# Optimization experiments

Hardware: AMD Instinct MI355X
Metric: run time of the kernel (lower is better)

## Reference

```python
import jax, jax.numpy as jnp
import numpy as np

HEADS = 16
DIM_HEAD = 64
DIM = 1024
INNER = HEADS * DIM_HEAD  # 1024
DIM_OUT = 1024


def setup_inputs() -> dict:
    key = jax.random.key(0)
    k1, k2, k3, k4 = jax.random.split(key, 4)
    B, N = 4, 2048
    x = jax.random.normal(k1, (B, N, DIM), dtype=jnp.float32)
    # hk.Linear(inner_dim*3, with_bias=False): weight shape [in, out]
    w_qkv = jax.random.normal(k2, (DIM, INNER * 3), dtype=jnp.float32) / np.sqrt(DIM)
    # hk.Linear(dim_out): weight [INNER, DIM_OUT] + bias
    w_out = jax.random.normal(k3, (INNER, DIM_OUT), dtype=jnp.float32) / np.sqrt(INNER)
    b_out = jax.random.normal(k4, (DIM_OUT,), dtype=jnp.float32) * 0.01
    return {"x": x, "w_qkv": w_qkv, "w_out": w_out, "b_out": b_out}


def reference(x, w_qkv, w_out, b_out):
    B, N, _ = x.shape
    scale = DIM_HEAD ** -0.5
    qkv = x @ w_qkv  # [B, N, 3*INNER]
    q, k, v = jnp.split(qkv, 3, axis=-1)
    # b n (h d) -> b h n d
    split_heads = lambda t: t.reshape(B, N, HEADS, DIM_HEAD).transpose(0, 2, 1, 3)
    q, k, v = split_heads(q), split_heads(k), split_heads(v)
    dots = jnp.einsum('bhid,bhjd->bhij', q, k) * scale  # [B, H, N, N]
    attn = jax.nn.softmax(dots, axis=-1)
    out = jnp.einsum('bhij,bhjd->bhid', attn, v)  # [B, H, N, D]
    out = out.transpose(0, 2, 1, 3).reshape(B, N, INNER)  # b h n d -> b n (h d)
    return out @ w_out + b_out
```

## Files before the change

kernel.cpp:

```cpp
#include <hip/hip_runtime.h>
#include <cstdint>


typedef unsigned short ushort_t;
typedef _Float16 half_t;
typedef half_t half8 __attribute__((ext_vector_type(8)));
typedef half_t half4 __attribute__((ext_vector_type(4)));
typedef float floatx4 __attribute__((ext_vector_type(4)));

__device__ __forceinline__ float bf2f(ushort_t h) {
  union { unsigned int u; float f; } v; v.u = ((unsigned int)h) << 16; return v.f;
}
__device__ __forceinline__ void async_copy16(const void* g, void* l) {
  __builtin_amdgcn_global_load_lds(
      reinterpret_cast<const __attribute__((address_space(1))) unsigned int*>(
          reinterpret_cast<uintptr_t>(g)),
      reinterpret_cast<__attribute__((address_space(3))) unsigned int*>(
          reinterpret_cast<uintptr_t>(l)),
      16, 0, 0);
}
__device__ __forceinline__ void vm_fence() {
  asm volatile("s_waitcnt vmcnt(0)" ::: "memory");
}

__global__ __launch_bounds__(256) void detect_dtype(const ushort_t* __restrict__ x,
                                                    int* __restrict__ flag) {
  __shared__ int cnt;
  if (threadIdx.x == 0) cnt = 0;
  __syncthreads();
  int local = 0;
  for (int i = threadIdx.x; i < 8192; i += 256)
    if ((x[i] & 0x7F80u) == 0x7F80u) ++local;
  atomicAdd(&cnt, local);
  __syncthreads();
  if (threadIdx.x == 0) *flag = (cnt >= 2) ? 1 : 0;
}

__global__ __launch_bounds__(256) void convert_to_f16(const void* __restrict__ src,
                                                      half_t* __restrict__ dst, int n,
                                                      const int* __restrict__ flag) {
  const int i0 = (blockIdx.x * 256 + threadIdx.x) * 4;
  if (i0 >= n) return;
  if (*flag) {
    const float* s = (const float*)src;
#pragma unroll
    for (int j = 0; j < 4; ++j) dst[i0 + j] = (half_t)s[i0 + j];
  } else {
    const ushort_t* s = (const ushort_t*)src;
#pragma unroll
    for (int j = 0; j < 4; ++j) dst[i0 + j] = (half_t)bf2f(s[i0 + j]);
  }
}

__global__ __launch_bounds__(256) void convert_bias(const void* __restrict__ src,
                                                    float* __restrict__ dst,
                                                    const int* __restrict__ flag) {
  const int i = blockIdx.x * 256 + threadIdx.x;
  if (i >= 1024) return;
  dst[i] = (*flag) ? ((const float*)src)[i] : bf2f(((const ushort_t*)src)[i]);
}

__global__ __launch_bounds__(256) void transpose_conv(const void* __restrict__ src,
                                                      half_t* __restrict__ dst, int R, int C,
                                                      const int* __restrict__ flag) {
  __shared__ half_t tile[64][65];
  const int c0 = blockIdx.x * 64, r0 = blockIdx.y * 64;
  const int tx = threadIdx.x & 63, ty = threadIdx.x >> 6;
  if (*flag) {
    const float* s = (const float*)src;
#pragma unroll
    for (int i = ty; i < 64; i += 4) tile[i][tx] = (half_t)s[(size_t)(r0 + i) * C + (c0 + tx)];
  } else {
    const ushort_t* s = (const ushort_t*)src;
#pragma unroll
    for (int i = ty; i < 64; i += 4) tile[i][tx] = (half_t)bf2f(s[(size_t)(r0 + i) * C + (c0 + tx)]);
  }
  __syncthreads();
#pragma unroll
  for (int i = ty; i < 64; i += 4) dst[(size_t)(c0 + i) * R + (r0 + tx)] = tile[tx][i];
}

__global__ __launch_bounds__(256) void gemm_qkv_kernel(
    const half_t* __restrict__ X, const half_t* __restrict__ WT,
    half_t* __restrict__ Qb, half_t* __restrict__ Kb, half_t* __restrict__ VTb) {
  __shared__ half_t smem[128 * 136];
  half_t* As = smem;
  half_t* Bs = smem + 128 * 64;
  const int tid = threadIdx.x;
  const int wv = tid >> 6, lane = tid & 63;
  const int l15 = lane & 15, quad = lane >> 4;
  const int l7 = l15 & 7;
  const int wm = wv & 1, wn = wv >> 1;
  const int nb = blockIdx.x, mb = blockIdx.y;
  const int rlo = lane >> 3, ci = lane & 7;
  const int sw_klo = (ci ^ rlo) * 8;

  floatx4 acc[4][4];
  const floatx4 z = {0.f, 0.f, 0.f, 0.f};
#pragma unroll
  for (int mi = 0; mi < 4; ++mi)
#pragma unroll
    for (int ni = 0; ni < 4; ++ni) acc[mi][ni] = z;

  const half_t* Abase = X + (size_t)mb * 128 * 1024;
  const half_t* Bbase = WT + (size_t)nb * 128 * 1024;

  for (int k0 = 0; k0 < 1024; k0 += 64) {
#pragma unroll
    for (int j = 0; j < 4; ++j) {
      const int rb = (wv * 4 + j) * 8;
      async_copy16(Abase + (size_t)(rb + rlo) * 1024 + k0 + sw_klo, &As[rb * 64]);
    }
#pragma unroll
    for (int j = 0; j < 4; ++j) {
      const int rb = (wv * 4 + j) * 8;
      async_copy16(Bbase + (size_t)(rb + rlo) * 1024 + k0 + sw_klo, &Bs[rb * 64]);
    }
    __syncthreads();
#pragma unroll
    for (int ks = 0; ks < 2; ++ks) {
      half8 af[4], bfv[4];
#pragma unroll
      for (int mi = 0; mi < 4; ++mi) {
        const int rr = wm * 64 + mi * 16 + l15;
        af[mi] = *(const half8*)&As[rr * 64 + (((ks * 4 + quad) ^ l7) * 8)];
      }
#pragma unroll
      for (int ni = 0; ni < 4; ++ni) {
        const int rr = wn * 64 + ni * 16 + l15;
        bfv[ni] = *(const half8*)&Bs[rr * 64 + (((ks * 4 + quad) ^ l7) * 8)];
      }
#pragma unroll
      for (int mi = 0; mi < 4; ++mi)
#pragma unroll
        for (int ni = 0; ni < 4; ++ni)
          acc[mi][ni] = __builtin_amdgcn_mfma_f32_16x16x32_f16(af[mi], bfv[ni], acc[mi][ni], 0, 0, 0);
    }
    __syncthreads();
  }

  const int which = nb >> 3;
  if (which != 2) {
#pragma unroll
    for (int mi = 0; mi < 4; ++mi) {
#pragma unroll
      for (int ni = 0; ni < 4; ++ni) {
        const int colg = nb * 128 + wn * 64 + ni * 16 + l15;
        const int hh = (colg & 1023) >> 6, dd = colg & 63;
#pragma unroll
        for (int r = 0; r < 4; ++r) {
          const int rowg = mb * 128 + wm * 64 + mi * 16 + quad * 4 + r;
          const int bb = rowg >> 11, nn = rowg & 2047;
          const half_t val = (half_t)acc[mi][ni][r];
          if (which == 0) Qb[((size_t)(bb * 16 + hh) * 2048 + nn) * 64 + dd] = val;
          else            Kb[((size_t)(bb * 16 + hh) * 2048 + nn) * 64 + dd] = val;
        }
      }
    }
  } else {
    const int nb2 = nb - 16;
#pragma unroll
    for (int mi = 0; mi < 4; ++mi)
#pragma unroll
      for (int ni = 0; ni < 4; ++ni) {
        const int nl = wn * 64 + ni * 16 + l15;
#pragma unroll
        for (int r = 0; r < 4; ++r) {
          const int ml = wm * 64 + mi * 16 + quad * 4 + r;
          smem[nl * 136 + ml] = (half_t)acc[mi][ni][r];
        }
      }
    __syncthreads();
    const int bb = mb >> 4;
    const int nn0 = (mb * 128) & 2047;
    const int lane2 = lane * 2;
#pragma unroll 4
    for (int it = 0; it < 32; ++it) {
      const int row = it * 4 + wv;
      const int hh = nb2 * 2 + (row >> 6);
      const int dd = row & 63;
      const uint32_t val = *(const uint32_t*)&smem[row * 136 + lane2];
      *(uint32_t*)&VTb[((size_t)((bb * 16 + hh) * 64 + dd)) * 2048 + nn0 + lane2] = val;
    }
  }
}

__global__ __launch_bounds__(256) void attn_kernel(
    const half_t* __restrict__ Qb, const half_t* __restrict__ Kb,
    const half_t* __restrict__ VTb, half_t* __restrict__ Ob) {
  __shared__ half_t smem[128 * 64];
  half_t* Ks = smem;
  half_t* VTs = smem + 64 * 64;
  const int tid = threadIdx.x, wv = tid >> 6, lane = tid & 63;
  const int l15 = lane & 15, quad = lane >> 4;
  const int l7 = l15 & 7;
  const int bid = blockIdx.x;
  const int xcd = bid & 7, idx = bid >> 3;
  const int bh = ((idx & 7) << 3) + xcd;
  const int qt = idx >> 3;
  const int bq = bh >> 4, hh = bh & 15;
  const half_t* Qg = Qb + (size_t)bh * 2048 * 64;
  const half_t* Kg = Kb + (size_t)bh * 2048 * 64;
  const half_t* Vg = VTb + (size_t)bh * 64 * 2048;
  const int q0 = qt * 128;
  const int rlo = lane >> 3, ci = lane & 7;
  const int sw_klo = (ci ^ rlo) * 8;
  const float C1 = 0.18033688011112043f;
  const float C2 = -5.770780163555854f;

#pragma unroll
  for (int j = 0; j < 4; ++j) {
    const int rb = (wv * 4 + j) * 8;
    async_copy16(Qg + (size_t)(q0 + rb + rlo) * 64 + sw_klo, &smem[rb * 64]);
  }
  vm_fence();
  half8 aq[2][2];
#pragma unroll
  for (int ks = 0; ks < 2; ++ks)
#pragma unroll
    for (int qi = 0; qi < 2; ++qi) {
      const int rr = wv * 32 + qi * 16 + l15;
      aq[ks][qi] = *(const half8*)&smem[rr * 64 + (((ks * 4 + quad) ^ l7) * 8)];
    }
  __syncthreads();

  floatx4 o_acc[2][4];
  const floatx4 z = {0.f, 0.f, 0.f, 0.f};
  float l_st[2] = {0.f, 0.f};
#pragma unroll
  for (int qi = 0; qi < 2; ++qi)
#pragma unroll
    for (int di = 0; di < 4; ++di) o_acc[qi][di] = z;

  for (int t = 0; t < 32; ++t) {
#pragma unroll
    for (int j = 0; j < 2; ++j) {
      const int rb = (wv * 2 + j) * 8;
      async_copy16(Kg + (size_t)(t * 64 + rb + rlo) * 64 + sw_klo, &Ks[rb * 64]);
    }
#pragma unroll
    for (int j = 0; j < 2; ++j) {
      const int db = (wv * 2 + j) * 8;
      async_copy16(Vg + (size_t)(db + rlo) * 2048 + t * 64 + sw_klo, &VTs[db * 64]);
    }
    __syncthreads();

    floatx4 s_acc[4][2];
#pragma unroll
    for (int ki = 0; ki < 4; ++ki)
#pragma unroll
      for (int qi = 0; qi < 2; ++qi) s_acc[ki][qi] = z;
#pragma unroll
    for (int ks = 0; ks < 2; ++ks) {
      half8 bk[4];
#pragma unroll
      for (int ki = 0; ki < 4; ++ki) {
        const int rr = ki * 16 + l15;
        bk[ki] = *(const half8*)&Ks[rr * 64 + (((ks * 4 + quad) ^ l7) * 8)];
      }
#pragma unroll
      for (int ki = 0; ki < 4; ++ki)
#pragma unroll
        for (int qi = 0; qi < 2; ++qi)
          s_acc[ki][qi] = __builtin_amdgcn_mfma_f32_16x16x32_f16(bk[ki], aq[ks][qi], s_acc[ki][qi], 0, 0, 0);
    }

#pragma unroll
    for (int ki = 0; ki < 4; ++ki)
#pragma unroll
      for (int qi = 0; qi < 2; ++qi) {
        float p0 = __builtin_amdgcn_exp2f(fmaf(s_acc[ki][qi][0], C1, C2));
        float p1 = __builtin_amdgcn_exp2f(fmaf(s_acc[ki][qi][1], C1, C2));
        float p2 = __builtin_amdgcn_exp2f(fmaf(s_acc[ki][qi][2], C1, C2));
        float p3 = __builtin_amdgcn_exp2f(fmaf(s_acc[ki][qi][3], C1, C2));
        s_acc[ki][qi][0] = p0; s_acc[ki][qi][1] = p1;
        s_acc[ki][qi][2] = p2; s_acc[ki][qi][3] = p3;
        l_st[qi] += (p0 + p1) + (p2 + p3);
      }

#pragma unroll
    for (int ki = 0; ki < 4; ++ki) {
      half4 ap[2];
#pragma unroll
      for (int qi = 0; qi < 2; ++qi) {
        ap[qi][0] = (half_t)s_acc[ki][qi][0];
        ap[qi][1] = (half_t)s_acc[ki][qi][1];
        ap[qi][2] = (half_t)s_acc[ki][qi][2];
        ap[qi][3] = (half_t)s_acc[ki][qi][3];
      }
      half4 bv[4];
#pragma unroll
      for (int di = 0; di < 4; ++di) {
        const int row = di * 16 + l15;
        bv[di] = *(const half4*)&VTs[row * 64 + (((ki * 2 + (quad >> 1)) ^ l7) * 8) + (quad & 1) * 4];
      }
#pragma unroll
      for (int qi = 0; qi < 2; ++qi)
#pragma unroll
        for (int di = 0; di < 4; ++di)
          o_acc[qi][di] = __builtin_amdgcn_mfma_f32_16x16x16f16(ap[qi], bv[di], o_acc[qi][di], 0, 0, 0);
    }
    __syncthreads();
  }

#pragma unroll
  for (int qi = 0; qi < 2; ++qi) {
    float rs = l_st[qi];
    rs += __shfl_xor(rs, 16);
    rs += __shfl_xor(rs, 32);
    l_st[qi] = 1.0f / rs;
  }
#pragma unroll
  for (int qi = 0; qi < 2; ++qi) {
#pragma unroll
    for (int r = 0; r < 4; ++r) {
      const float inv = __shfl(l_st[qi], quad * 4 + r);
      const int nn = q0 + wv * 32 + qi * 16 + quad * 4 + r;
#pragma unroll
      for (int di = 0; di < 4; ++di)
        Ob[((size_t)(bq * 2048 + nn)) * 1024 + hh * 64 + di * 16 + l15] =
            (half_t)(o_acc[qi][di][r] * inv);
    }
  }
}

__global__ __launch_bounds__(256) void gemm_out_kernel(
    const half_t* __restrict__ A, const half_t* __restrict__ WT,
    const float* __restrict__ bias, float* __restrict__ out) {
  __shared__ half_t As[128 * 64];
  __shared__ half_t Bs[128 * 64];
  const int tid = threadIdx.x;
  const int wv = tid >> 6, lane = tid & 63;
  const int l15 = lane & 15, quad = lane >> 4;
  const int l7 = l15 & 7;
  const int wm = wv & 1, wn = wv >> 1;
  const int nb = blockIdx.x, mb = blockIdx.y;
  const int rlo = lane >> 3, ci = lane & 7;
  const int sw_klo = (ci ^ rlo) * 8;

  floatx4 acc[4][4];
  const floatx4 z = {0.f, 0.f, 0.f, 0.f};
#pragma unroll
  for (int mi = 0; mi < 4; ++mi)
#pragma unroll
    for (int ni = 0; ni < 4; ++ni) acc[mi][ni] = z;

  const half_t* Abase = A + (size_t)mb * 128 * 1024;
  const half_t* Bbase = WT + (size_t)nb * 128 * 1024;

  for (int k0 = 0; k0 < 1024; k0 += 64) {
#pragma unroll
    for (int j = 0; j < 4; ++j) {
      const int rb = (wv * 4 + j) * 8;
      async_copy16(Abase + (size_t)(rb + rlo) * 1024 + k0 + sw_klo, &As[rb * 64]);
    }
#pragma unroll
    for (int j = 0; j < 4; ++j) {
      const int rb = (wv * 4 + j) * 8;
      async_copy16(Bbase + (size_t)(rb + rlo) * 1024 + k0 + sw_klo, &Bs[rb * 64]);
    }
    __syncthreads();
#pragma unroll
    for (int ks = 0; ks < 2; ++ks) {
      half8 af[4], bfv[4];
#pragma unroll
      for (int mi = 0; mi < 4; ++mi) {
        const int rr = wm * 64 + mi * 16 + l15;
        af[mi] = *(const half8*)&As[rr * 64 + (((ks * 4 + quad) ^ l7) * 8)];
      }
#pragma unroll
      for (int ni = 0; ni < 4; ++ni) {
        const int rr = wn * 64 + ni * 16 + l15;
        bfv[ni] = *(const half8*)&Bs[rr * 64 + (((ks * 4 + quad) ^ l7) * 8)];
      }
#pragma unroll
      for (int mi = 0; mi < 4; ++mi)
#pragma unroll
        for (int ni = 0; ni < 4; ++ni)
          acc[mi][ni] = __builtin_amdgcn_mfma_f32_16x16x32_f16(af[mi], bfv[ni], acc[mi][ni], 0, 0, 0);
    }
    __syncthreads();
  }

#pragma unroll
  for (int mi = 0; mi < 4; ++mi) {
#pragma unroll
    for (int ni = 0; ni < 4; ++ni) {
      const int colg = nb * 128 + wn * 64 + ni * 16 + l15;
      const float bs = bias[colg];
#pragma unroll
      for (int r = 0; r < 4; ++r) {
        const int rowg = mb * 128 + wm * 64 + mi * 16 + quad * 4 + r;
        out[(size_t)rowg * 1024 + colg] = acc[mi][ni][r] + bs;
      }
    }
  }
}

extern "C" void kernel_launch(void* const* d_in, const int* in_sizes, int n_in,
                              void* d_out, int out_size, void* d_ws, size_t ws_size,
                              hipStream_t stream) {
  const void* x_raw     = d_in[0];
  const void* w_qkv_raw = d_in[1];
  const void* w_out_raw = d_in[2];
  const void* b_out_raw = d_in[3];
  float* out = (float*)d_out;

  char* ws = (char*)d_ws;
  half_t* xb    = (half_t*)(ws);
  half_t* Qb    = (half_t*)(ws + ((size_t)16 << 20));
  half_t* Kb    = (half_t*)(ws + ((size_t)32 << 20));
  half_t* VTb   = (half_t*)(ws + ((size_t)48 << 20));
  half_t* WTqkv = (half_t*)(ws + ((size_t)64 << 20));
  half_t* WTout = (half_t*)(ws + ((size_t)70 << 20));
  float*  bb    = (float*)(ws + ((size_t)72 << 20));
  int*    flag  = (int*)(ws + ((size_t)72 << 20) + 8192);
  half_t* Ob    = xb;

  detect_dtype<<<1, 256, 0, stream>>>((const ushort_t*)x_raw, flag);
  convert_to_f16<<<8192, 256, 0, stream>>>(x_raw, xb, 8192 * 1024, flag);
  convert_bias<<<4, 256, 0, stream>>>(b_out_raw, bb, flag);
  transpose_conv<<<dim3(48, 16), 256, 0, stream>>>(w_qkv_raw, WTqkv, 1024, 3072, flag);
  transpose_conv<<<dim3(16, 16), 256, 0, stream>>>(w_out_raw, WTout, 1024, 1024, flag);
  gemm_qkv_kernel<<<dim3(24, 64), 256, 0, stream>>>(xb, WTqkv, Qb, Kb, VTb);
  attn_kernel<<<1024, 256, 0, stream>>>(Qb, Kb, VTb, Ob);
  gemm_out_kernel<<<dim3(8, 64), 256, 0, stream>>>(Ob, WTout, bb, out);
}
```

Measured before the change: 308.1 us.

## Double-buffer K/V tiles in attention and stage epilogue stores through LDS

The attention kernel now double-buffers K and V^T tiles in a larger shared buffer and prefetches tile t+1 while computing tile t. This removes one barrier per iteration and hides global load latency. The softmax scale is folded into Q in the QKV GEMM epilogue, and P is converted with packed fp16 conversion. The Q/K and attention output epilogues stage results through LDS to write coalesced 32-bit stores, and V^T stores are permuted to match a new bank-conflict-avoiding read pattern. The risks are higher LDS usage per block, which may lower occupancy, and correctness depends on the V permutation matching on both the write and read sides.

New measurement: 317.3 us. 3.0% more time.

```diff
diff --git a/kernel.cpp b/kernel.cpp
--- a/kernel.cpp
+++ b/kernel.cpp
@@ -6,7 +6,10 @@
 typedef _Float16 half_t;
 typedef half_t half8 __attribute__((ext_vector_type(8)));
 typedef half_t half4 __attribute__((ext_vector_type(4)));
+typedef __fp16 fp16x2 __attribute__((ext_vector_type(2)));
 typedef float floatx4 __attribute__((ext_vector_type(4)));
+
+#define QSCALE 0.18033688011112043f
 
 __device__ __forceinline__ float bf2f(ushort_t h) {
   union { unsigned int u; float f; } v; v.u = ((unsigned int)h) << 16; return v.f;
@@ -18,6 +21,9 @@
       reinterpret_cast<__attribute__((address_space(3))) unsigned int*>(
           reinterpret_cast<uintptr_t>(l)),
       16, 0, 0);
+}
+__device__ __forceinline__ void lds_fence() {
+  asm volatile("s_waitcnt lgkmcnt(0)" ::: "memory");
 }
 __device__ __forceinline__ void vm_fence() {
   asm volatile("s_waitcnt vmcnt(0)" ::: "memory");
@@ -68,15 +74,12 @@
   const int tx = threadIdx.x & 63, ty = threadIdx.x >> 6;
   if (*flag) {
     const float* s = (const float*)src;
-#pragma unroll
     for (int i = ty; i < 64; i += 4) tile[i][tx] = (half_t)s[(size_t)(r0 + i) * C + (c0 + tx)];
   } else {
     const ushort_t* s = (const ushort_t*)src;
-#pragma unroll
     for (int i = ty; i < 64; i += 4) tile[i][tx] = (half_t)bf2f(s[(size_t)(r0 + i) * C + (c0 + tx)]);
   }
   __syncthreads();
-#pragma unroll
   for (int i = ty; i < 64; i += 4) dst[(size_t)(c0 + i) * R + (r0 + tx)] = tile[tx][i];
 }
 
@@ -141,21 +144,31 @@
 
   const int which = nb >> 3;
   if (which != 2) {
-#pragma unroll
-    for (int mi = 0; mi < 4; ++mi) {
+    const float sc = (which == 0) ? QSCALE : 1.0f;
+#pragma unroll
+    for (int mi = 0; mi < 4; ++mi)
 #pragma unroll
       for (int ni = 0; ni < 4; ++ni) {
-        const int colg = nb * 128 + wn * 64 + ni * 16 + l15;
-        const int hh = (colg & 1023) >> 6, dd = colg & 63;
+        const int col = wn * 64 + ni * 16 + l15;
 #pragma unroll
         for (int r = 0; r < 4; ++r) {
-          const int rowg = mb * 128 + wm * 64 + mi * 16 + quad * 4 + r;
-          const int bb = rowg >> 11, nn = rowg & 2047;
-          const half_t val = (half_t)acc[mi][ni][r];
-          if (which == 0) Qb[((size_t)(bb * 16 + hh) * 2048 + nn) * 64 + dd] = val;
-          else            Kb[((size_t)(bb * 16 + hh) * 2048 + nn) * 64 + dd] = val;
+          const int row = wm * 64 + mi * 16 + quad * 4 + r;
+          smem[row * 132 + col] = (half_t)(acc[mi][ni][r] * sc);
         }
       }
+    __syncthreads();
+    half_t* dstB = (which == 0) ? Qb : Kb;
+    const int hbase = (nb & 7) * 2;
+    const int c2 = lane * 2;
+    const int hh = hbase + (c2 >> 6);
+    const int dd = c2 & 63;
+#pragma unroll 4
+    for (int i = 0; i < 32; ++i) {
+      const int row = wv * 32 + i;
+      const uint32_t val = *(const uint32_t*)&smem[row * 132 + c2];
+      const int rowg = mb * 128 + row;
+      const int bb = rowg >> 11, nn = rowg & 2047;
+      *(uint32_t*)&dstB[(((size_t)(bb * 16 + hh)) * 2048 + nn) * 64 + dd] = val;
     }
   } else {
     const int nb2 = nb - 16;
@@ -179,8 +192,9 @@
       const int row = it * 4 + wv;
       const int hh = nb2 * 2 + (row >> 6);
       const int dd = row & 63;
+      const int keyoff = lane2 ^ ((dd & 8) ? 4 : 0);
       const uint32_t val = *(const uint32_t*)&smem[row * 136 + lane2];
-      *(uint32_t*)&VTb[((size_t)((bb * 16 + hh) * 64 + dd)) * 2048 + nn0 + lane2] = val;
+      *(uint32_t*)&VTb[((size_t)((bb * 16 + hh) * 64 + dd)) * 2048 + nn0 + keyoff] = val;
     }
   }
 }
@@ -188,9 +202,7 @@
 __global__ __launch_bounds__(256) void attn_kernel(
     const half_t* __restrict__ Qb, const half_t* __restrict__ Kb,
     const half_t* __restrict__ VTb, half_t* __restrict__ Ob) {
-  __shared__ half_t smem[128 * 64];
-  half_t* Ks = smem;
-  half_t* VTs = smem + 64 * 64;
+  __shared__ half_t smem[16384];
   const int tid = threadIdx.x, wv = tid >> 6, lane = tid & 63;
   const int l15 = lane & 15, quad = lane >> 4;
   const int l7 = l15 & 7;
@@ -205,8 +217,14 @@
   const int q0 = qt * 128;
   const int rlo = lane >> 3, ci = lane & 7;
   const int sw_klo = (ci ^ rlo) * 8;
-  const float C1 = 0.18033688011112043f;
-  const float C2 = -5.770780163555854f;
+
+  const int q1 = quad >> 1, qb0 = quad & 1, b3 = (l15 >> 3) & 1;
+  int kx[2], vx[4];
+#pragma unroll
+  for (int ks = 0; ks < 2; ++ks) kx[ks] = ((ks * 4 + quad) ^ l7) * 8;
+#pragma unroll
+  for (int ki = 0; ki < 4; ++ki)
+    vx[ki] = (((ki * 2 + q1) ^ l7) * 8) + ((qb0 ^ b3) * 4);
 
 #pragma unroll
   for (int j = 0; j < 4; ++j) {
@@ -232,18 +250,39 @@
 #pragma unroll
     for (int di = 0; di < 4; ++di) o_acc[qi][di] = z;
 
-  for (int t = 0; t < 32; ++t) {
+  {
 #pragma unroll
     for (int j = 0; j < 2; ++j) {
       const int rb = (wv * 2 + j) * 8;
-      async_copy16(Kg + (size_t)(t * 64 + rb + rlo) * 64 + sw_klo, &Ks[rb * 64]);
+      async_copy16(Kg + (size_t)(rb + rlo) * 64 + sw_klo, &smem[rb * 64]);
     }
 #pragma unroll
     for (int j = 0; j < 2; ++j) {
       const int db = (wv * 2 + j) * 8;
-      async_copy16(Vg + (size_t)(db + rlo) * 2048 + t * 64 + sw_klo, &VTs[db * 64]);
-    }
-    __syncthreads();
+      async_copy16(Vg + (size_t)(db + rlo) * 2048 + sw_klo, &smem[8192 + db * 64]);
+    }
+  }
+
+  for (int t = 0; t < 32; ++t) {
+    const int co = (t & 1) * 4096;
+    const int po = 4096 - co;
+    __syncthreads();
+    if (t < 31) {
+#pragma unroll
+      for (int j = 0; j < 2; ++j) {
+        const int rb = (wv * 2 + j) * 8;
+        async_copy16(Kg + (size_t)((t + 1) * 64 + rb + rlo) * 64 + sw_klo,
+                     &smem[po + rb * 64]);
+      }
+#pragma unroll
+      for (int j = 0; j < 2; ++j) {
+        const int db = (wv * 2 + j) * 8;
+        async_copy16(Vg + (size_t)(db + rlo) * 2048 + (t + 1) * 64 + sw_klo,
+                     &smem[8192 + po + db * 64]);
+      }
+    }
+    const half_t* Kc = &smem[co];
+    const half_t* Vc = &smem[8192 + co];
 
     floatx4 s_acc[4][2];
 #pragma unroll
@@ -254,10 +293,8 @@
     for (int ks = 0; ks < 2; ++ks) {
       half8 bk[4];
 #pragma unroll
-      for (int ki = 0; ki < 4; ++ki) {
-        const int rr = ki * 16 + l15;
-        bk[ki] = *(const half8*)&Ks[rr * 64 + (((ks * 4 + quad) ^ l7) * 8)];
-      }
+      for (int ki = 0; ki < 4; ++ki)
+        bk[ki] = *(const half8*)&Kc[(ki * 16 + l15) * 64 + kx[ks]];
 #pragma unroll
       for (int ki = 0; ki < 4; ++ki)
 #pragma unroll
@@ -265,62 +302,67 @@
           s_acc[ki][qi] = __builtin_amdgcn_mfma_f32_16x16x32_f16(bk[ki], aq[ks][qi], s_acc[ki][qi], 0, 0, 0);
     }
 
+    half4 ap[4][2];
 #pragma unroll
     for (int ki = 0; ki < 4; ++ki)
 #pragma unroll
       for (int qi = 0; qi < 2; ++qi) {
-        float p0 = __builtin_amdgcn_exp2f(fmaf(s_acc[ki][qi][0], C1, C2));
-        float p1 = __builtin_amdgcn_exp2f(fmaf(s_acc[ki][qi][1], C1, C2));
-        float p2 = __builtin_amdgcn_exp2f(fmaf(s_acc[ki][qi][2], C1, C2));
-        float p3 = __builtin_amdgcn_exp2f(fmaf(s_acc[ki][qi][3], C1, C2));
-        s_acc[ki][qi][0] = p0; s_acc[ki][qi][1] = p1;
-        s_acc[ki][qi][2] = p2; s_acc[ki][qi][3] = p3;
+        const float p0 = __builtin_amdgcn_exp2f(s_acc[ki][qi][0]);
+        const float p1 = __builtin_amdgcn_exp2f(s_acc[ki][qi][1]);
+        const float p2 = __builtin_amdgcn_exp2f(s_acc[ki][qi][2]);
+        const float p3 = __builtin_amdgcn_exp2f(s_acc[ki][qi][3]);
         l_st[qi] += (p0 + p1) + (p2 + p3);
+        union { fp16x2 v; uint32_t u; } lo_, hi_;
+        lo_.v = __builtin_amdgcn_cvt_pkrtz(p0, p1);
+        hi_.v = __builtin_amdgcn_cvt_pkrtz(p2, p3);
+        union { uint32_t u[2]; half4 h; } a_;
+        a_.u[0] = lo_.u; a_.u[1] = hi_.u;
+        ap[ki][qi] = a_.h;
       }
 
 #pragma unroll
     for (int ki = 0; ki < 4; ++ki) {
-      half4 ap[2];
-#pragma unroll
-      for (int qi = 0; qi < 2; ++qi) {
-        ap[qi][0] = (half_t)s_acc[ki][qi][0];
-        ap[qi][1] = (half_t)s_acc[ki][qi][1];
-        ap[qi][2] = (half_t)s_acc[ki][qi][2];
-        ap[qi][3] = (half_t)s_acc[ki][qi][3];
-      }
       half4 bv[4];
 #pragma unroll
-      for (int di = 0; di < 4; ++di) {
-        const int row = di * 16 + l15;
-        bv[di] = *(const half4*)&VTs[row * 64 + (((ki * 2 + (quad >> 1)) ^ l7) * 8) + (quad & 1) * 4];
-      }
+      for (int di = 0; di < 4; ++di)
+        bv[di] = *(const half4*)&Vc[(di * 16 + l15) * 64 + vx[ki]];
 #pragma unroll
       for (int qi = 0; qi < 2; ++qi)
 #pragma unroll
         for (int di = 0; di < 4; ++di)
-          o_acc[qi][di] = __builtin_amdgcn_mfma_f32_16x16x16f16(ap[qi], bv[di], o_acc[qi][di], 0, 0, 0);
-    }
-    __syncthreads();
-  }
-
+          o_acc[qi][di] = __builtin_amdgcn_mfma_f32_16x16x16f16(ap[ki][qi], bv[di], o_acc[qi][di], 0, 0, 0);
+    }
+  }
+
+  float linv[2];
 #pragma unroll
   for (int qi = 0; qi < 2; ++qi) {
     float rs = l_st[qi];
     rs += __shfl_xor(rs, 16);
     rs += __shfl_xor(rs, 32);
-    l_st[qi] = 1.0f / rs;
-  }
-#pragma unroll
-  for (int qi = 0; qi < 2; ++qi) {
+    linv[qi] = 1.0f / rs;
+  }
+
+  __syncthreads();
+#pragma unroll
+  for (int qi = 0; qi < 2; ++qi)
 #pragma unroll
     for (int r = 0; r < 4; ++r) {
-      const float inv = __shfl(l_st[qi], quad * 4 + r);
-      const int nn = q0 + wv * 32 + qi * 16 + quad * 4 + r;
+      const float inv = __shfl(linv[qi], quad * 4 + r);
+      const int row = wv * 32 + qi * 16 + quad * 4 + r;
 #pragma unroll
       for (int di = 0; di < 4; ++di)
-        Ob[((size_t)(bq * 2048 + nn)) * 1024 + hh * 64 + di * 16 + l15] =
-            (half_t)(o_acc[qi][di][r] * inv);
-    }
+        smem[row * 72 + di * 16 + l15] = (half_t)(o_acc[qi][di][r] * inv);
+    }
+  lds_fence();
+  const int c2 = (lane & 31) * 2;
+  const int rsel = lane >> 5;
+#pragma unroll 4
+  for (int i = 0; i < 16; ++i) {
+    const int row = wv * 32 + i * 2 + rsel;
+    const uint32_t val = *(const uint32_t*)&smem[row * 72 + c2];
+    const int nn = q0 + row;
+    *(uint32_t*)&Ob[((size_t)(bq * 2048 + nn)) * 1024 + hh * 64 + c2] = val;
   }
 }
 
```
